# Optimization experiments

Hardware: AMD Instinct MI355X
Metric: run time of the kernel (lower is better)

The kernel has to match this reference:

```python
import jax, jax.numpy as jnp
import numpy as np

N, CS, CZ = 512, 384, 128
H, C, PQ, PV = 12, 16, 4, 8
NB = 8
EPS = 1e-8


def _ln(x, g, b):
    m = jnp.mean(x, axis=-1, keepdims=True)
    v = jnp.mean((x - m) ** 2, axis=-1, keepdims=True)
    return (x - m) / jnp.sqrt(v + 1e-5) * g + b


def _quat_rot(bcd):
    # (1, b, c, d) quaternion -> rotation matrix, as in AF2 BackboneUpdate
    ones = jnp.ones(bcd.shape[:-1] + (1,), bcd.dtype)
    q = jnp.concatenate([ones, bcd], axis=-1)
    q = q / jnp.linalg.norm(q, axis=-1, keepdims=True)
    w, x, y, z = q[..., 0], q[..., 1], q[..., 2], q[..., 3]
    R = jnp.stack([
        1 - 2 * (y * y + z * z), 2 * (x * y - w * z), 2 * (x * z + w * y),
        2 * (x * y + w * z), 1 - 2 * (x * x + z * z), 2 * (y * z - w * x),
        2 * (x * z - w * y), 2 * (y * z + w * x), 1 - 2 * (x * x + y * y),
    ], axis=-1)
    return R.reshape(bcd.shape[:-1] + (3, 3))


def _ipa(s, z, R, t, p):
    n = s.shape[0]
    q = (s @ p['w_q']).reshape(n, H, C)
    kv = (s @ p['w_kv']).reshape(n, H, 2, C)
    k, v = kv[..., 0, :], kv[..., 1, :]

    # local points -> global frames
    q_pts = (s @ p['w_qpts']).reshape(n, H * PQ, 3)
    q_pts = jnp.einsum('nxy,npy->npx', R, q_pts) + t[:, None, :]
    q_pts = q_pts.reshape(n, H, PQ, 3)
    kv_pts = (s @ p['w_kvpts']).reshape(n, H * (PQ + PV), 3)
    kv_pts = jnp.einsum('nxy,npy->npx', R, kv_pts) + t[:, None, :]
    kv_pts = kv_pts.reshape(n, H, PQ + PV, 3)
    k_pts, v_pts = kv_pts[:, :, :PQ], kv_pts[:, :, PQ:]

    b = z @ p['w_b']  # [i, j, H]

    scalar = jnp.einsum('ihc,jhc->hij', q, k) / np.sqrt(C)
    # sum_p ||q_ip - k_jp||^2 expanded to avoid [N,N,H,P,3] intermediate
    sq_q = jnp.sum(q_pts ** 2, axis=(-1, -2)).T  # [H, i]
    sq_k = jnp.sum(k_pts ** 2, axis=(-1, -2)).T  # [H, j]
    cross = jnp.einsum('ihpc,jhpc->hij', q_pts, k_pts)
    d2 = sq_q[:, :, None] + sq_k[:, None, :] - 2.0 * cross  # [H, i, j]

    gamma = jax.nn.softplus(p['head_weights'])  # [H]
    w_C = np.sqrt(2.0 / (9.0 * PQ))
    w_L = np.sqrt(1.0 / 3.0)
    logits = w_L * (scalar + jnp.transpose(b, (2, 0, 1))
                    - gamma[:, None, None] * (w_C / 2.0) * d2)
    a = jax.nn.softmax(logits, axis=-1)  # [H, i, j]

    o = jnp.einsum('hij,jhc->ihc', a, v).reshape(n, H * C)
    o_pt = jnp.einsum('hij,jhpc->ihpc', a, v_pts)
    # back to local frame: R_i^{-1} (o_pt - t_i)
    o_pt = jnp.einsum('nyx,nhpy->nhpx', R, o_pt - t[:, None, None, :])
    o_pt_norm = jnp.sqrt(jnp.sum(o_pt ** 2, axis=-1) + EPS)  # [n, H, PV]
    o_pair = jnp.einsum('hij,ijz->ihz', a, z).reshape(n, H * CZ)

    cat = jnp.concatenate([o, o_pt.reshape(n, H * PV * 3),
                           o_pt_norm.reshape(n, H * PV), o_pair], axis=-1)
    return cat @ p['w_out'] + p['b_out']


def _forward(s, z, p):
    n = s.shape[0]
    R = jnp.broadcast_to(jnp.eye(3, dtype=s.dtype), (n, 3, 3))
    t = jnp.zeros((n, 3), s.dtype)
    for _ in range(NB):  # shared weights across blocks, as in AF2
        s = s + _ipa(s, z, R, t, p)
        s = _ln(s, p['ln1_g'], p['ln1_b'])
        h = jax.nn.relu(s @ p['w_t1'])
        h = jax.nn.relu(h @ p['w_t2'])
        s = s + h @ p['w_t3']
        s = _ln(s, p['ln2_g'], p['ln2_b'])
        upd = s @ p['w_bb'] + p['b_bb']  # [n, 6]
        Ru = _quat_rot(upd[:, :3])
        tu = upd[:, 3:]
        t = jnp.einsum('nxy,ny->nx', R, tu) + t
        R = jnp.einsum('nxy,nyz->nxz', R, Ru)
    return jnp.concatenate([s, t], axis=-1)  # [n, CS + 3]


def setup_inputs() -> dict:
    key = jax.random.key(0)
    ks = jax.random.split(key, 12)
    sc = 0.02
    cat_dim = H * C + H * PV * 3 + H * PV + H * CZ  # 2112
    return {
        's': jax.random.normal(ks[0], (N, CS), jnp.float32),
        'z': jax.random.normal(ks[1], (N, N, CZ), jnp.float32),
        'w_q': jax.random.normal(ks[2], (CS, H * C), jnp.float32) * sc,
        'w_kv': jax.random.normal(ks[3], (CS, H * 2 * C), jnp.float32) * sc,
        'w_qpts': jax.random.normal(ks[4], (CS, H * PQ * 3), jnp.float32) * sc,
        'w_kvpts': jax.random.normal(ks[5], (CS, H * (PQ + PV) * 3), jnp.float32) * sc,
        'w_b': jax.random.normal(ks[6], (CZ, H), jnp.float32) * sc,
        'head_weights': jnp.zeros((H,), jnp.float32),
        'w_out': jax.random.normal(ks[7], (cat_dim, CS), jnp.float32) * sc,
        'b_out': jnp.zeros((CS,), jnp.float32),
        'ln1_g': jnp.ones((CS,), jnp.float32),
        'ln1_b': jnp.zeros((CS,), jnp.float32),
        'w_t1': jax.random.normal(ks[8], (CS, CS), jnp.float32) * sc,
        'w_t2': jax.random.normal(ks[9], (CS, CS), jnp.float32) * sc,
        'w_t3': jax.random.normal(ks[10], (CS, CS), jnp.float32) * sc,
        'ln2_g': jnp.ones((CS,), jnp.float32),
        'ln2_b': jnp.zeros((CS,), jnp.float32),
        'w_bb': jax.random.normal(ks[11], (CS, 6), jnp.float32) * sc,
        'b_bb': jnp.zeros((6,), jnp.float32),
    }


def reference(s, z, w_q, w_kv, w_qpts, w_kvpts, w_b, head_weights, w_out,
              b_out, ln1_g, ln1_b, w_t1, w_t2, w_t3, ln2_g, ln2_b, w_bb, b_bb):
    p = dict(w_q=w_q, w_kv=w_kv, w_qpts=w_qpts, w_kvpts=w_kvpts, w_b=w_b,
             head_weights=head_weights, w_out=w_out, b_out=b_out,
             ln1_g=ln1_g, ln1_b=ln1_b, w_t1=w_t1, w_t2=w_t2, w_t3=w_t3,
             ln2_g=ln2_g, ln2_b=ln2_b, w_bb=w_bb, b_bb=b_bb)
    return _forward(s, z, p)
```

## Files before the change

### kernel.cpp

```cpp
#include <hip/hip_runtime.h>
#include <hip/hip_bf16.h>

constexpr int Nres = 512;
constexpr int Cs   = 384;
constexpr int Cz   = 128;
constexpr int NH   = 12;
constexpr int HC   = 16;
constexpr int NPQ  = 4;
constexpr int NPV  = 8;
constexpr int NBLK = 8;
constexpr int PROJD = NH*HC + NH*2*HC + NH*NPQ*3 + NH*(NPQ+NPV)*3;
constexpr int CATD = NH*HC + NH*NPV*3 + NH*NPV + NH*Cz;
constexpr float W_L  = 0.57735026918962576f;
constexpr float W_C2 = 0.11785113019775793f;

using u16 = unsigned short;
typedef __bf16 bf16x8 __attribute__((ext_vector_type(8)));
typedef float  f32x4  __attribute__((ext_vector_type(4)));

static inline int gdiv(int n, int b) { return (n + b - 1) / b; }

static __device__ __forceinline__ u16 f2bf(float x) {
    __hip_bfloat16 h = __float2bfloat16(x);
    return *reinterpret_cast<u16*>(&h);
}
static __device__ __forceinline__ float bf2f(u16 x) {
    return __bfloat162float(*reinterpret_cast<__hip_bfloat16*>(&x));
}

__global__ void k_init(const float* __restrict__ s_in, float* __restrict__ s_cur,
                       u16* __restrict__ s_bf,
                       float* __restrict__ R, float* __restrict__ t) {
    int idx = blockIdx.x * blockDim.x + threadIdx.x;
    if (idx < Nres * Cs) { float v = s_in[idx]; s_cur[idx] = v; s_bf[idx] = f2bf(v); }
    if (idx < Nres * 9) {
        int e = idx % 9;
        R[idx] = (e == 0 || e == 4 || e == 8) ? 1.f : 0.f;
    }
    if (idx < Nres * 3) t[idx] = 0.f;
}

__global__ void k_concatW(const float* __restrict__ w_q, const float* __restrict__ w_kv,
                          const float* __restrict__ w_qpts, const float* __restrict__ w_kvpts,
                          float* __restrict__ Wcat) {
    int idx = blockIdx.x * blockDim.x + threadIdx.x;
    if (idx >= Cs * PROJD) return;
    int k = idx / PROJD, n = idx - k * PROJD;
    float v;
    if      (n < 192) v = w_q[k * 192 + n];
    else if (n < 576) v = w_kv[k * 384 + (n - 192)];
    else if (n < 720) v = w_qpts[k * 144 + (n - 576)];
    else              v = w_kvpts[k * 432 + (n - 720)];
    Wcat[idx] = v;
}

__global__ void k_transposeW(const float* __restrict__ in, u16* __restrict__ out,
                             int K, int N) {
    __shared__ float tile[32][33];
    int n0 = blockIdx.x * 32, k0 = blockIdx.y * 32;
    int tx = threadIdx.x & 31, ty = threadIdx.x >> 5;
#pragma unroll
    for (int j = 0; j < 4; j++)
        tile[ty + j * 8][tx] = in[(size_t)(k0 + ty + j * 8) * N + n0 + tx];
    __syncthreads();
#pragma unroll
    for (int j = 0; j < 4; j++)
        out[(size_t)(n0 + ty + j * 8) * K + k0 + tx] = f2bf(tile[tx][ty + j * 8]);
}

__global__ void k_zT(const float* __restrict__ z, u16* __restrict__ zT) {
    __shared__ float tile[32][33];
    int i  = blockIdx.x;
    int j0 = blockIdx.y * 32;
    int c0 = blockIdx.z * 32;
    int tx = threadIdx.x & 31, ty = threadIdx.x >> 5;
    const float* src = z + (size_t)i * Nres * Cz;
#pragma unroll
    for (int l = 0; l < 4; l++)
        tile[ty + l * 8][tx] = src[(size_t)(j0 + ty + l * 8) * Cz + c0 + tx];
    __syncthreads();
    u16* dst = zT + (size_t)i * Cz * Nres;
#pragma unroll
    for (int l = 0; l < 4; l++)
        dst[(size_t)(c0 + ty + l * 8) * Nres + j0 + tx] = f2bf(tile[tx][ty + l * 8]);
}

__global__ void __launch_bounds__(256)
k_gemm_mfma(const u16* __restrict__ A, const u16* __restrict__ Bt,
            float* __restrict__ P, int M, int K, int N, int Kc) {
    __shared__ u16 As[2][64 * 40];
    __shared__ u16 Bs[2][64 * 40];
    const int tid = threadIdx.x;
    const int m0 = blockIdx.y * 64;
    const int n0 = blockIdx.x * 64;
    const int kbeg = blockIdx.z * Kc;
    const int kend = kbeg + Kc;
    const int wv = tid >> 6, lane = tid & 63;
    const int wm = (wv >> 1) * 32, wn = (wv & 1) * 32;
    const int lrow = lane & 15, lq = lane >> 4;

    f32x4 zero = {0.f, 0.f, 0.f, 0.f};
    f32x4 acc00 = zero, acc01 = zero, acc10 = zero, acc11 = zero;

    const int srow = tid >> 2;
    const int sko  = (tid & 3) * 8;
    const size_t aoff = (size_t)(m0 + srow) * K + sko;
    const size_t boff = (size_t)(n0 + srow) * K + sko;

    uint4 ra = *(const uint4*)&A[aoff + kbeg];
    uint4 rb = *(const uint4*)&Bt[boff + kbeg];
    *(uint4*)&As[0][srow * 40 + sko] = ra;
    *(uint4*)&Bs[0][srow * 40 + sko] = rb;
    __syncthreads();

    int buf = 0;
    for (int k0 = kbeg; k0 < kend; k0 += 32) {
        const bool nxt = (k0 + 32 < kend);
        if (nxt) {
            ra = *(const uint4*)&A[aoff + k0 + 32];
            rb = *(const uint4*)&Bt[boff + k0 + 32];
        }
        bf16x8 a0 = *reinterpret_cast<const bf16x8*>(&As[buf][(wm + lrow) * 40 + lq * 8]);
        bf16x8 a1 = *reinterpret_cast<const bf16x8*>(&As[buf][(wm + 16 + lrow) * 40 + lq * 8]);
        bf16x8 b0 = *reinterpret_cast<const bf16x8*>(&Bs[buf][(wn + lrow) * 40 + lq * 8]);
        bf16x8 b1 = *reinterpret_cast<const bf16x8*>(&Bs[buf][(wn + 16 + lrow) * 40 + lq * 8]);
        acc00 = __builtin_amdgcn_mfma_f32_16x16x32_bf16(a0, b0, acc00, 0, 0, 0);
        acc01 = __builtin_amdgcn_mfma_f32_16x16x32_bf16(a0, b1, acc01, 0, 0, 0);
        acc10 = __builtin_amdgcn_mfma_f32_16x16x32_bf16(a1, b0, acc10, 0, 0, 0);
        acc11 = __builtin_amdgcn_mfma_f32_16x16x32_bf16(a1, b1, acc11, 0, 0, 0);
        if (nxt) {
            *(uint4*)&As[buf ^ 1][srow * 40 + sko] = ra;
            *(uint4*)&Bs[buf ^ 1][srow * 40 + sko] = rb;
            __syncthreads();
            buf ^= 1;
        }
    }
    float* Pp = P + (size_t)blockIdx.z * M * N;
    const int rbase = m0 + wm + lq * 4;
    const int cbase = n0 + wn + lrow;
#pragma unroll
    for (int r = 0; r < 4; r++) {
        Pp[(size_t)(rbase + r) * N + cbase]           = acc00[r];
        Pp[(size_t)(rbase + r) * N + cbase + 16]      = acc01[r];
        Pp[(size_t)(rbase + 16 + r) * N + cbase]      = acc10[r];
        Pp[(size_t)(rbase + 16 + r) * N + cbase + 16] = acc11[r];
    }
}

__global__ void __launch_bounds__(256)
k_gemm_proj(const u16* __restrict__ A, const u16* __restrict__ Bt,
            float* __restrict__ outT, int M, int K, int N) {
    __shared__ u16 As[2][32 * 40];
    __shared__ u16 Bs[2][64 * 40];
    const int tid = threadIdx.x;
    const int m0 = blockIdx.y * 32;
    const int n0 = blockIdx.x * 64;
    const int wv = tid >> 6, lane = tid & 63;
    const int wm = (wv >> 1) * 16, wn = (wv & 1) * 32;
    const int lrow = lane & 15, lq = lane >> 4;
    f32x4 zero = {0.f, 0.f, 0.f, 0.f};
    f32x4 acc0 = zero, acc1 = zero;
    const int srow = tid >> 2, sko = (tid & 3) * 8;
    const size_t aoff = (size_t)(m0 + srow) * K + sko;
    const size_t boff = (size_t)(n0 + srow) * K + sko;

    uint4 ra, rb;
    if (tid < 128) ra = *(const uint4*)&A[aoff];
    rb = *(const uint4*)&Bt[boff];
    if (tid < 128) *(uint4*)&As[0][srow * 40 + sko] = ra;
    *(uint4*)&Bs[0][srow * 40 + sko] = rb;
    __syncthreads();

    int buf = 0;
    for (int k0 = 0; k0 < K; k0 += 32) {
        const bool nxt = (k0 + 32 < K);
        if (nxt) {
            if (tid < 128) ra = *(const uint4*)&A[aoff + k0 + 32];
            rb = *(const uint4*)&Bt[boff + k0 + 32];
        }
        bf16x8 a  = *reinterpret_cast<const bf16x8*>(&As[buf][(wm + lrow) * 40 + lq * 8]);
        bf16x8 b0 = *reinterpret_cast<const bf16x8*>(&Bs[buf][(wn + lrow) * 40 + lq * 8]);
        bf16x8 b1 = *reinterpret_cast<const bf16x8*>(&Bs[buf][(wn + 16 + lrow) * 40 + lq * 8]);
        acc0 = __builtin_amdgcn_mfma_f32_16x16x32_bf16(a, b0, acc0, 0, 0, 0);
        acc1 = __builtin_amdgcn_mfma_f32_16x16x32_bf16(a, b1, acc1, 0, 0, 0);
        if (nxt) {
            if (tid < 128) *(uint4*)&As[buf ^ 1][srow * 40 + sko] = ra;
            *(uint4*)&Bs[buf ^ 1][srow * 40 + sko] = rb;
            __syncthreads();
            buf ^= 1;
        }
    }
    const int rbase = m0 + wm + lq * 4;
    const int cbase = n0 + wn + lrow;
    *reinterpret_cast<f32x4*>(&outT[(size_t)cbase * M + rbase])        = acc0;
    *reinterpret_cast<f32x4*>(&outT[(size_t)(cbase + 16) * M + rbase]) = acc1;
}

__global__ void __launch_bounds__(256)
k_gemm_tr(const u16* __restrict__ Abf, const float* __restrict__ As0,
          const float* __restrict__ As1, const u16* __restrict__ Bt,
          float* __restrict__ Pout, int amode) {
    __shared__ u16 Asm[2][32 * 40];
    __shared__ u16 Bsm[2][64 * 40];
    const int tid = threadIdx.x;
    const int m0 = blockIdx.y * 32;
    const int n0 = blockIdx.x * 64;
    const int kbeg = blockIdx.z * 192;
    const int kend = kbeg + 192;
    const int wv = tid >> 6, lane = tid & 63;
    const int wm = (wv >> 1) * 16, wn = (wv & 1) * 32;
    const int lrow = lane & 15, lq = lane >> 4;
    f32x4 zero = {0.f, 0.f, 0.f, 0.f};
    f32x4 acc0 = zero, acc1 = zero;
    const int srow = tid >> 2, sko = (tid & 3) * 8;
    const int rowR = tid >> 3, c4 = (tid & 7) * 4;
    const size_t aoffb = (size_t)(m0 + srow) * Cs + sko;
    const size_t aoffr = (size_t)(m0 + rowR) * Cs + c4;
    const size_t boff  = (size_t)(n0 + srow) * Cs + sko;

    uint4 ra, rb;
    float4 f0, f1;
    rb = *(const uint4*)&Bt[boff + kbeg];
    if (amode == 0) { if (tid < 128) ra = *(const uint4*)&Abf[aoffb + kbeg]; }
    else { f0 = *(const float4*)&As0[aoffr + kbeg]; f1 = *(const float4*)&As1[aoffr + kbeg]; }

    if (amode == 0) { if (tid < 128) *(uint4*)&Asm[0][srow * 40 + sko] = ra; }
    else {
        uint2 wp;
        wp.x = (unsigned)f2bf(fmaxf(f0.x + f1.x, 0.f)) | ((unsigned)f2bf(fmaxf(f0.y + f1.y, 0.f)) << 16);
        wp.y = (unsigned)f2bf(fmaxf(f0.z + f1.z, 0.f)) | ((unsigned)f2bf(fmaxf(f0.w + f1.w, 0.f)) << 16);
        *(uint2*)&Asm[0][rowR * 40 + c4] = wp;
    }
    *(uint4*)&Bsm[0][srow * 40 + sko] = rb;
    __syncthreads();

    int buf = 0;
    for (int k0 = kbeg; k0 < kend; k0 += 32) {
        const bool nxt = (k0 + 32 < kend);
        if (nxt) {
            rb = *(const uint4*)&Bt[boff + k0 + 32];
            if (amode == 0) { if (tid < 128) ra = *(const uint4*)&Abf[aoffb + k0 + 32]; }
            else { f0 = *(const float4*)&As0[aoffr + k0 + 32]; f1 = *(const float4*)&As1[aoffr + k0 + 32]; }
        }
        bf16x8 a  = *reinterpret_cast<const bf16x8*>(&Asm[buf][(wm + lrow) * 40 + lq * 8]);
        bf16x8 b0 = *reinterpret_cast<const bf16x8*>(&Bsm[buf][(wn + lrow) * 40 + lq * 8]);
        bf16x8 b1 = *reinterpret_cast<const bf16x8*>(&Bsm[buf][(wn + 16 + lrow) * 40 + lq * 8]);
        acc0 = __builtin_amdgcn_mfma_f32_16x16x32_bf16(a, b0, acc0, 0, 0, 0);
        acc1 = __builtin_amdgcn_mfma_f32_16x16x32_bf16(a, b1, acc1, 0, 0, 0);
        if (nxt) {
            if (amode == 0) { if (tid < 128) *(uint4*)&Asm[buf ^ 1][srow * 40 + sko] = ra; }
            else {
                uint2 wp;
                wp.x = (unsigned)f2bf(fmaxf(f0.x + f1.x, 0.f)) | ((unsigned)f2bf(fmaxf(f0.y + f1.y, 0.f)) << 16);
                wp.y = (unsigned)f2bf(fmaxf(f0.z + f1.z, 0.f)) | ((unsigned)f2bf(fmaxf(f0.w + f1.w, 0.f)) << 16);
                *(uint2*)&Asm[buf ^ 1][rowR * 40 + c4] = wp;
            }
            *(uint4*)&Bsm[buf ^ 1][srow * 40 + sko] = rb;
            __syncthreads();
            buf ^= 1;
        }
    }
    float* Pp = Pout + (size_t)blockIdx.z * Nres * Cs;
    const int rbase = m0 + wm + lq * 4;
    const int cbase = n0 + wn + lrow;
#pragma unroll
    for (int r = 0; r < 4; r++) {
        Pp[(size_t)(rbase + r) * Cs + cbase]      = acc0[r];
        Pp[(size_t)(rbase + r) * Cs + cbase + 16] = acc1[r];
    }
}

__global__ void k_bproj(const float* __restrict__ z, const float* __restrict__ w_b,
                        u16* __restrict__ b_hij_bf) {
    __shared__ float zs[16][129];
    __shared__ float wbs[Cz * NH];
    const int tid = threadIdx.x;
    const int base = blockIdx.x * 16;
#pragma unroll
    for (int l = 0; l < 6; l++) {
        int idx = tid + l * 256;
        if (idx < Cz * NH) wbs[idx] = w_b[idx];
    }
#pragma unroll
    for (int l = 0; l < 8; l++) {
        int idx = tid + l * 256;
        int r = idx >> 7, c = idx & 127;
        zs[r][c] = z[(size_t)(base + r) * Cz + c];
    }
    __syncthreads();
    if (tid < 192) {
        int h = tid >> 4, r = tid & 15;
        float acc = 0.f;
        for (int c = 0; c < Cz; c++) acc += zs[r][c] * wbs[c * NH + h];
        int row = base + r;
        int i = row >> 9, j = row & 511;
        b_hij_bf[((size_t)h * Nres + i) * Nres + j] = f2bf(acc * W_L);
    }
}

__global__ void k_prep(const float* __restrict__ projT, const float* __restrict__ R,
                       const float* __restrict__ t, const float* __restrict__ hw,
                       u16* __restrict__ Aaug, u16* __restrict__ Baug,
                       u16* __restrict__ vhT) {
    int idx = blockIdx.x * blockDim.x + threadIdx.x;
    if (idx >= NH * Nres) return;
    int h = idx / Nres, i = idx % Nres;
#define PR(col) projT[(size_t)(col) * Nres + i]
    float R_[9], t_[3];
#pragma unroll
    for (int e = 0; e < 9; e++) R_[e] = R[i * 9 + e];
#pragma unroll
    for (int e = 0; e < 3; e++) t_[e] = t[i * 3 + e];
    float gam = log1pf(__expf(hw[h]));
    float ch  = sqrtf(2.f * gam * W_C2);

    u16 arow[32], brow[32];
#pragma unroll
    for (int c = 0; c < HC; c++) {
        arow[c] = f2bf(PR(h * HC + c) * (W_L * 0.25f));
        brow[c] = f2bf(PR(192 + h * 2 * HC + c));
        vhT[((size_t)h * 48 + c) * Nres + i] = f2bf(PR(192 + h * 2 * HC + HC + c));
    }
#pragma unroll
    for (int p = 0; p < NPQ; p++) {
        int c0 = 576 + (h * NPQ + p) * 3;
        float y0 = PR(c0 + 0), y1 = PR(c0 + 1), y2 = PR(c0 + 2);
        float v0 = R_[0]*y0 + R_[1]*y1 + R_[2]*y2 + t_[0];
        float v1 = R_[3]*y0 + R_[4]*y1 + R_[5]*y2 + t_[1];
        float v2 = R_[6]*y0 + R_[7]*y1 + R_[8]*y2 + t_[2];
        float s = W_L * ch;
        arow[16 + p*3 + 0] = f2bf(v0 * s);
        arow[16 + p*3 + 1] = f2bf(v1 * s);
        arow[16 + p*3 + 2] = f2bf(v2 * s);
    }
    float sk = 0.f;
#pragma unroll
    for (int p = 0; p < NPQ + NPV; p++) {
        int c0 = 720 + (h * (NPQ+NPV) + p) * 3;
        float y0 = PR(c0 + 0), y1 = PR(c0 + 1), y2 = PR(c0 + 2);
        float v0 = R_[0]*y0 + R_[1]*y1 + R_[2]*y2 + t_[0];
        float v1 = R_[3]*y0 + R_[4]*y1 + R_[5]*y2 + t_[1];
        float v2 = R_[6]*y0 + R_[7]*y1 + R_[8]*y2 + t_[2];
        if (p < NPQ) {
            brow[16 + p*3 + 0] = f2bf(v0 * ch);
            brow[16 + p*3 + 1] = f2bf(v1 * ch);
            brow[16 + p*3 + 2] = f2bf(v2 * ch);
            sk += v0*v0 + v1*v1 + v2*v2;
        } else {
            int cc = 16 + (p - NPQ) * 3;
            vhT[((size_t)h * 48 + cc + 0) * Nres + i] = f2bf(v0);
            vhT[((size_t)h * 48 + cc + 1) * Nres + i] = f2bf(v1);
            vhT[((size_t)h * 48 + cc + 2) * Nres + i] = f2bf(v2);
        }
    }
#undef PR
    float x = -W_L * gam * W_C2 * sk;
    u16 hi = f2bf(x);
    float lo = x - bf2f(hi);
    arow[28] = f2bf(1.0f); arow[29] = f2bf(1.0f); arow[30] = 0; arow[31] = 0;
    brow[28] = hi;         brow[29] = f2bf(lo);   brow[30] = 0; brow[31] = 0;

    uint4* ad = (uint4*)&Aaug[((size_t)h * Nres + i) * 32];
    uint4* bd = (uint4*)&Baug[((size_t)h * Nres + i) * 32];
    const uint4* as = (const uint4*)arow;
    const uint4* bs = (const uint4*)brow;
#pragma unroll
    for (int e = 0; e < 4; e++) { ad[e] = as[e]; bd[e] = bs[e]; }
}

__global__ void __launch_bounds__(256)
k_attn(const u16* __restrict__ Aaug, const u16* __restrict__ Baug,
       const u16* __restrict__ b_hij_bf, const u16* __restrict__ vhT,
       const float* __restrict__ R, const float* __restrict__ t,
       u16* __restrict__ Pbf, u16* __restrict__ cat_bf) {
    __shared__ u16 P_lds[16 * 520];
    __shared__ float Ctp[4][16 * 49];
    __shared__ float sred[4][32];

    const int i0 = blockIdx.x * 16;
    const int h  = blockIdx.y;
    const int tid = threadIdx.x;
    const int w = tid >> 6, lane = tid & 63;
    const int lrow = lane & 15, lq = lane >> 4;
    const int jbase = w * 128;

    const u16* bhp = b_hij_bf + ((size_t)h * Nres + i0) * Nres;
    uint4 bhreg[4];
#pragma unroll
    for (int l = 0; l < 4; l++) {
        int v = tid + l * 256;
        int rr = v >> 6, cq = v & 63;
        bhreg[l] = *(const uint4*)&bhp[(size_t)rr * Nres + cq * 8];
    }

    bf16x8 afrag = *reinterpret_cast<const bf16x8*>(
        &Aaug[((size_t)h * Nres + i0 + lrow) * 32 + lq * 8]);
    f32x4 zero = {0.f, 0.f, 0.f, 0.f};
    f32x4 acc[8];
#pragma unroll
    for (int tt = 0; tt < 8; tt++) {
        bf16x8 bfr = *reinterpret_cast<const bf16x8*>(
            &Baug[((size_t)h * Nres + jbase + tt * 16 + lrow) * 32 + lq * 8]);
        acc[tt] = __builtin_amdgcn_mfma_f32_16x16x32_bf16(afrag, bfr, zero, 0, 0, 0);
    }

#pragma unroll
    for (int l = 0; l < 4; l++) {
        int v = tid + l * 256;
        int rr = v >> 6, cq = v & 63;
        *(uint4*)&P_lds[rr * 520 + cq * 8] = bhreg[l];
    }
    __syncthreads();
#pragma unroll
    for (int tt = 0; tt < 8; tt++)
#pragma unroll
        for (int r = 0; r < 4; r++)
            acc[tt][r] += bf2f(P_lds[(lq * 4 + r) * 520 + jbase + tt * 16 + lrow]);

    float pmx[4] = {-1e30f, -1e30f, -1e30f, -1e30f};
#pragma unroll
    for (int tt = 0; tt < 8; tt++)
#pragma unroll
        for (int r = 0; r < 4; r++) pmx[r] = fmaxf(pmx[r], acc[tt][r]);
#pragma unroll
    for (int off = 8; off > 0; off >>= 1)
#pragma unroll
        for (int r = 0; r < 4; r++) pmx[r] = fmaxf(pmx[r], __shfl_xor(pmx[r], off));
    if (lrow == 0) {
#pragma unroll
        for (int r = 0; r < 4; r++) sred[w][lq * 4 + r] = pmx[r];
    }
    __syncthreads();
    float mx[4];
#pragma unroll
    for (int r = 0; r < 4; r++) {
        int row = lq * 4 + r;
        mx[r] = fmaxf(fmaxf(sred[0][row], sred[1][row]), fmaxf(sred[2][row], sred[3][row]));
    }
    float psm[4] = {0.f, 0.f, 0.f, 0.f};
#pragma unroll
    for (int tt = 0; tt < 8; tt++)
#pragma unroll
        for (int r = 0; r < 4; r++) { acc[tt][r] = __expf(acc[tt][r] - mx[r]); psm[r] += acc[tt][r]; }
#pragma unroll
    for (int off = 8; off > 0; off >>= 1)
#pragma unroll
        for (int r = 0; r < 4; r++) psm[r] += __shfl_xor(psm[r], off);
    if (lrow == 0) {
#pragma unroll
        for (int r = 0; r < 4; r++) sred[w][16 + lq * 4 + r] = psm[r];
    }
    __syncthreads();
    float inv[4];
#pragma unroll
    for (int r = 0; r < 4; r++) {
        int row = 16 + lq * 4 + r;
        inv[r] = 1.f / (sred[0][row] + sred[1][row] + sred[2][row] + sred[3][row]);
    }

#pragma unroll
    for (int tt = 0; tt < 8; tt++)
#pragma unroll
        for (int r = 0; r < 4; r++)
            P_lds[(lq * 4 + r) * 520 + jbase + tt * 16 + lrow] = f2bf(acc[tt][r] * inv[r]);
    __syncthreads();

#pragma unroll
    for (int l = 0; l < 4; l++) {
        int v = tid + l * 256;
        int rr = v >> 6, cq = v & 63;
        *(uint4*)&Pbf[((size_t)h * Nres + i0 + rr) * 512 + cq * 8] =
            *(const uint4*)&P_lds[rr * 520 + cq * 8];
    }

    const u16* Bvp = vhT + (size_t)h * 48 * Nres;
    f32x4 o0 = zero, o1 = zero, o2 = zero;
#pragma unroll
    for (int s = 0; s < 4; s++) {
        int k0 = w * 128 + s * 32;
        bf16x8 a  = *reinterpret_cast<const bf16x8*>(&P_lds[lrow * 520 + k0 + lq * 8]);
        bf16x8 b0 = *reinterpret_cast<const bf16x8*>(&Bvp[(size_t)(lrow) * Nres + k0 + lq * 8]);
        bf16x8 b1 = *reinterpret_cast<const bf16x8*>(&Bvp[(size_t)(16 + lrow) * Nres + k0 + lq * 8]);
        bf16x8 b2 = *reinterpret_cast<const bf16x8*>(&Bvp[(size_t)(32 + lrow) * Nres + k0 + lq * 8]);
        o0 = __builtin_amdgcn_mfma_f32_16x16x32_bf16(a, b0, o0, 0, 0, 0);
        o1 = __builtin_amdgcn_mfma_f32_16x16x32_bf16(a, b1, o1, 0, 0, 0);
        o2 = __builtin_amdgcn_mfma_f32_16x16x32_bf16(a, b2, o2, 0, 0, 0);
    }
#pragma unroll
    for (int r = 0; r < 4; r++) {
        int row = lq * 4 + r;
        Ctp[w][row * 49 + lrow]      = o0[r];
        Ctp[w][row * 49 + 16 + lrow] = o1[r];
        Ctp[w][row * 49 + 32 + lrow] = o2[r];
    }
    __syncthreads();

    {
        int r = tid >> 4, c = tid & 15;
        float v = Ctp[0][r * 49 + c] + Ctp[1][r * 49 + c] + Ctp[2][r * 49 + c] + Ctp[3][r * 49 + c];
        cat_bf[(size_t)(i0 + r) * CATD + h * HC + c] = f2bf(v);
    }
    if (tid < 128) {
        int r = tid >> 3, p = tid & 7;
        int i = i0 + r;
        float g0 = 0.f, g1 = 0.f, g2 = 0.f;
#pragma unroll
        for (int ww = 0; ww < 4; ww++) {
            g0 += Ctp[ww][r * 49 + 16 + p * 3 + 0];
            g1 += Ctp[ww][r * 49 + 16 + p * 3 + 1];
            g2 += Ctp[ww][r * 49 + 16 + p * 3 + 2];
        }
        float d0 = g0 - t[i * 3 + 0], d1 = g1 - t[i * 3 + 1], d2v = g2 - t[i * 3 + 2];
        const float* Rn = R + i * 9;
        float l0 = Rn[0] * d0 + Rn[3] * d1 + Rn[6] * d2v;
        float l1 = Rn[1] * d0 + Rn[4] * d1 + Rn[7] * d2v;
        float l2 = Rn[2] * d0 + Rn[5] * d1 + Rn[8] * d2v;
        int hp = h * NPV + p;
        u16* crow = cat_bf + (size_t)i * CATD;
        crow[192 + hp * 3 + 0] = f2bf(l0);
        crow[192 + hp * 3 + 1] = f2bf(l1);
        crow[192 + hp * 3 + 2] = f2bf(l2);
        crow[480 + hp] = f2bf(sqrtf(l0 * l0 + l1 * l1 + l2 * l2 + 1e-8f));
    }
}

__global__ void __launch_bounds__(256)
k_opair(const u16* __restrict__ Pbf, const u16* __restrict__ zT,
        u16* __restrict__ cat_bf) {
    __shared__ u16 P_lds[16 * 520];
    __shared__ u16 Bs[2][128 * 40];
    const int i = blockIdx.x;
    const int tid = threadIdx.x;
    const int wv = tid >> 6, ln = tid & 63;
    const int srow = tid >> 2, sko = (tid & 3) * 8;
    const u16* Bp = zT + (size_t)i * Cz * Nres;
    const size_t b0off = (size_t)srow * Nres + sko;
    const size_t b1off = (size_t)(64 + srow) * Nres + sko;

    uint4 rb0 = *(const uint4*)&Bp[b0off];
    uint4 rb1 = *(const uint4*)&Bp[b1off];

#pragma unroll
    for (int l = 0; l < 3; l++) {
        int v = tid + l * 256;
        int hh = v >> 6, cq = v & 63;
        *(uint4*)&P_lds[hh * 520 + cq * 8] =
            *(const uint4*)&Pbf[((size_t)hh * Nres + i) * 512 + cq * 8];
    }
    for (int l = tid; l < 4 * 520; l += 256) P_lds[12 * 520 + l] = 0;

    *(uint4*)&Bs[0][srow * 40 + sko]        = rb0;
    *(uint4*)&Bs[0][(64 + srow) * 40 + sko] = rb1;
    __syncthreads();

    const int lrow = ln & 15, lq = ln >> 4;
    const int wn = wv * 32;
    f32x4 zero = {0.f, 0.f, 0.f, 0.f};
    f32x4 acc0 = zero, acc1 = zero;
    int buf = 0;
    for (int k0 = 0; k0 < Nres; k0 += 32) {
        const bool nxt = (k0 + 32 < Nres);
        if (nxt) {
            rb0 = *(const uint4*)&Bp[b0off + k0 + 32];
            rb1 = *(const uint4*)&Bp[b1off + k0 + 32];
        }
        bf16x8 a  = *reinterpret_cast<const bf16x8*>(&P_lds[lrow * 520 + k0 + lq * 8]);
        bf16x8 b0 = *reinterpret_cast<const bf16x8*>(&Bs[buf][(wn + lrow) * 40 + lq * 8]);
        bf16x8 b1 = *reinterpret_cast<const bf16x8*>(&Bs[buf][(wn + 16 + lrow) * 40 + lq * 8]);
        acc0 = __builtin_amdgcn_mfma_f32_16x16x32_bf16(a, b0, acc0, 0, 0, 0);
        acc1 = __builtin_amdgcn_mfma_f32_16x16x32_bf16(a, b1, acc1, 0, 0, 0);
        if (nxt) {
            *(uint4*)&Bs[buf ^ 1][srow * 40 + sko]        = rb0;
            *(uint4*)&Bs[buf ^ 1][(64 + srow) * 40 + sko] = rb1;
            __syncthreads();
            buf ^= 1;
        }
    }
    u16* crow = cat_bf + (size_t)i * CATD + 576;
#pragma unroll
    for (int r = 0; r < 4; r++) {
        int row = lq * 4 + r;
        if (row < NH) {
            crow[row * Cz + wn + lrow]      = f2bf(acc0[r]);
            crow[row * Cz + wn + 16 + lrow] = f2bf(acc1[r]);
        }
    }
}

__global__ void k_reduce_ln(const float* __restrict__ P, const float* __restrict__ bias,
                            float* __restrict__ s, u16* __restrict__ s_bf,
                            const float* __restrict__ g, const float* __restrict__ b,
                            int nsplit) {
    __shared__ float red[512];
    int i = blockIdx.x, tid = threadIdx.x;
    float v = s[(size_t)i * Cs + tid];
    if (bias) v += bias[tid];
    for (int sp = 0; sp < nsplit; sp++) v += P[(size_t)sp * Nres * Cs + (size_t)i * Cs + tid];
    red[tid] = v;
    if (tid < 128) red[384 + tid] = 0.f;
    __syncthreads();
    for (int st = 256; st > 0; st >>= 1) { if (tid < st) red[tid] += red[tid + st]; __syncthreads(); }
    float mean = red[0] / Cs;
    __syncthreads();
    float d = v - mean;
    red[tid] = d * d;
    if (tid < 128) red[384 + tid] = 0.f;
    __syncthreads();
    for (int st = 256; st > 0; st >>= 1) { if (tid < st) red[tid] += red[tid + st]; __syncthreads(); }
    float var = red[0] / Cs;
    float o = d * rsqrtf(var + 1e-5f) * g[tid] + b[tid];
    s[(size_t)i * Cs + tid] = o;
    s_bf[(size_t)i * Cs + tid] = f2bf(o);
}

__global__ void k_reduce_ln_bb(const float* __restrict__ P, float* __restrict__ s,
                               u16* __restrict__ s_bf,
                               const float* __restrict__ g, const float* __restrict__ b,
                               int nsplit,
                               const float* __restrict__ w_bb, const float* __restrict__ b_bb,
                               float* __restrict__ R, float* __restrict__ t,
                               float* __restrict__ outbuf) {
    __shared__ float red[512];
    __shared__ float uw[36];
    int i = blockIdx.x, tid = threadIdx.x;
    float v = s[(size_t)i * Cs + tid];
    for (int sp = 0; sp < nsplit; sp++) v += P[(size_t)sp * Nres * Cs + (size_t)i * Cs + tid];
    red[tid] = v;
    if (tid < 128) red[384 + tid] = 0.f;
    __syncthreads();
    for (int st = 256; st > 0; st >>= 1) { if (tid < st) red[tid] += red[tid + st]; __syncthreads(); }
    float mean = red[0] / Cs;
    __syncthreads();
    float d = v - mean;
    red[tid] = d * d;
    if (tid < 128) red[384 + tid] = 0.f;
    __syncthreads();
    for (int st = 256; st > 0; st >>= 1) { if (tid < st) red[tid] += red[tid + st]; __syncthreads(); }
    float var = red[0] / Cs;
    float o = d * rsqrtf(var + 1e-5f) * g[tid] + b[tid];
    s[(size_t)i * Cs + tid] = o;
    s_bf[(size_t)i * Cs + tid] = f2bf(o);
    if (outbuf) outbuf[(size_t)i * (Cs + 3) + tid] = o;

    float u[6];
#pragma unroll
    for (int dd = 0; dd < 6; dd++) u[dd] = o * w_bb[tid * 6 + dd];
#pragma unroll
    for (int off = 32; off > 0; off >>= 1)
#pragma unroll
        for (int dd = 0; dd < 6; dd++) u[dd] += __shfl_xor(u[dd], off);
    int wv = tid >> 6, lane = tid & 63;
    if (lane == 0) {
#pragma unroll
        for (int dd = 0; dd < 6; dd++) uw[wv * 6 + dd] = u[dd];
    }
    __syncthreads();
    if (tid == 0) {
        float uu[6];
#pragma unroll
        for (int dd = 0; dd < 6; dd++) {
            float a = b_bb[dd];
            for (int w = 0; w < 6; w++) a += uw[w * 6 + dd];
            uu[dd] = a;
        }
        float qb = uu[0], qc = uu[1], qd = uu[2];
        float inv = rsqrtf(1.f + qb*qb + qc*qc + qd*qd);
        float w = inv, x = qb * inv, y = qc * inv, zq = qd * inv;
        float Ru[9] = {
            1.f - 2.f*(y*y + zq*zq), 2.f*(x*y - w*zq),       2.f*(x*zq + w*y),
            2.f*(x*y + w*zq),        1.f - 2.f*(x*x + zq*zq), 2.f*(y*zq - w*x),
            2.f*(x*zq - w*y),        2.f*(y*zq + w*x),        1.f - 2.f*(x*x + y*y)
        };
        float Ro[9];
#pragma unroll
        for (int e = 0; e < 9; e++) Ro[e] = R[i * 9 + e];
        float tu0 = uu[3], tu1 = uu[4], tu2 = uu[5];
        float t0 = t[i*3+0] + Ro[0]*tu0 + Ro[1]*tu1 + Ro[2]*tu2;
        float t1 = t[i*3+1] + Ro[3]*tu0 + Ro[4]*tu1 + Ro[5]*tu2;
        float t2 = t[i*3+2] + Ro[6]*tu0 + Ro[7]*tu1 + Ro[8]*tu2;
        t[i*3+0] = t0; t[i*3+1] = t1; t[i*3+2] = t2;
        if (outbuf) {
            outbuf[(size_t)i * (Cs + 3) + Cs + 0] = t0;
            outbuf[(size_t)i * (Cs + 3) + Cs + 1] = t1;
            outbuf[(size_t)i * (Cs + 3) + Cs + 2] = t2;
        }
#pragma unroll
        for (int r = 0; r < 3; r++)
#pragma unroll
            for (int c = 0; c < 3; c++)
                R[i*9 + r*3 + c] = Ro[r*3+0]*Ru[0*3+c] + Ro[r*3+1]*Ru[1*3+c] + Ro[r*3+2]*Ru[2*3+c];
    }
}

extern "C" void kernel_launch(void* const* d_in, const int* in_sizes, int n_in,
                              void* d_out, int out_size, void* d_ws, size_t ws_size,
                              hipStream_t stream) {
    const float* s_in    = (const float*)d_in[0];
    const float* z       = (const float*)d_in[1];
    const float* w_q     = (const float*)d_in[2];
    const float* w_kv    = (const float*)d_in[3];
    const float* w_qpts  = (const float*)d_in[4];
    const float* w_kvpts = (const float*)d_in[5];
    const float* w_b     = (const float*)d_in[6];
    const float* hw      = (const float*)d_in[7];
    const float* w_out   = (const float*)d_in[8];
    const float* b_out   = (const float*)d_in[9];
    const float* ln1_g   = (const float*)d_in[10];
    const float* ln1_b   = (const float*)d_in[11];
    const float* w_t1    = (const float*)d_in[12];
    const float* w_t2    = (const float*)d_in[13];
    const float* w_t3    = (const float*)d_in[14];
    const float* ln2_g   = (const float*)d_in[15];
    const float* ln2_b   = (const float*)d_in[16];
    const float* w_bb    = (const float*)d_in[17];
    const float* b_bb    = (const float*)d_in[18];
    float* out = (float*)d_out;

    float* ws = (float*)d_ws;
    size_t off = 0;
    float* s_cur = ws + off; off += (size_t)Nres * Cs;
    float* projT = ws + off; off += (size_t)Nres * PROJD;
    float* Wcat  = ws + off; off += (size_t)Cs * PROJD;
    float* Rbuf  = ws + off; off += (size_t)Nres * 9;
    float* tbuf  = ws + off; off += (size_t)Nres * 3;
    float* Pslab = ws + off; off += (size_t)11 * Nres * Cs;
    u16* b_hij_bf = (u16*)(ws + off); off += (size_t)NH * Nres * Nres / 2;
    u16* s_bf   = (u16*)(ws + off); off += (size_t)Nres * Cs / 2;
    u16* cat_bf = (u16*)(ws + off); off += (size_t)Nres * CATD / 2;
    u16* WcatT  = (u16*)(ws + off); off += (size_t)Cs * PROJD / 2;
    u16* w_outT = (u16*)(ws + off); off += (size_t)CATD * Cs / 2;
    u16* w_t1T  = (u16*)(ws + off); off += (size_t)Cs * Cs / 2;
    u16* w_t2T  = (u16*)(ws + off); off += (size_t)Cs * Cs / 2;
    u16* w_t3T  = (u16*)(ws + off); off += (size_t)Cs * Cs / 2;
    u16* Pbf    = (u16*)(ws + off); off += (size_t)NH * Nres * Nres / 2;
    u16* vhTbf  = (u16*)(ws + off); off += (size_t)NH * 48 * Nres / 2;
    u16* Aaug   = (u16*)(ws + off); off += (size_t)NH * Nres * 32 / 2;
    u16* Baug   = (u16*)(ws + off); off += (size_t)NH * Nres * 32 / 2;
    u16* zTbf   = (u16*)(ws + off); off += (size_t)Nres * Cz * Nres / 2;

    const int MNs = Nres * Cs;

    k_init<<<gdiv(Nres*Cs, 256), 256, 0, stream>>>(s_in, s_cur, s_bf, Rbuf, tbuf);
    k_concatW<<<gdiv(Cs*PROJD, 256), 256, 0, stream>>>(w_q, w_kv, w_qpts, w_kvpts, Wcat);
    k_transposeW<<<dim3(PROJD/32, Cs/32), 256, 0, stream>>>(Wcat, WcatT, Cs, PROJD);
    k_transposeW<<<dim3(Cs/32, CATD/32), 256, 0, stream>>>(w_out, w_outT, CATD, Cs);
    k_transposeW<<<dim3(Cs/32, Cs/32), 256, 0, stream>>>(w_t1, w_t1T, Cs, Cs);
    k_transposeW<<<dim3(Cs/32, Cs/32), 256, 0, stream>>>(w_t2, w_t2T, Cs, Cs);
    k_transposeW<<<dim3(Cs/32, Cs/32), 256, 0, stream>>>(w_t3, w_t3T, Cs, Cs);
    k_bproj<<<Nres*Nres/16, 256, 0, stream>>>(z, w_b, b_hij_bf);
    k_zT<<<dim3(Nres, Nres/32, Cz/32), 256, 0, stream>>>(z, zTbf);

    for (int it = 0; it < NBLK; it++) {
        k_gemm_proj<<<dim3(PROJD/64, Nres/32), 256, 0, stream>>>(s_bf, WcatT, projT, Nres, Cs, PROJD);
        k_prep<<<gdiv(NH*Nres, 256), 256, 0, stream>>>(projT, Rbuf, tbuf, hw, Aaug, Baug, vhTbf);
        k_attn<<<dim3(Nres/16, NH), 256, 0, stream>>>(Aaug, Baug, b_hij_bf, vhTbf, Rbuf, tbuf, Pbf, cat_bf);
        k_opair<<<Nres, 256, 0, stream>>>(Pbf, zTbf, cat_bf);
        k_gemm_mfma<<<dim3(Cs/64, Nres/64, 6), 256, 0, stream>>>(cat_bf, w_outT, Pslab, Nres, CATD, Cs, 352);
        k_reduce_ln<<<Nres, Cs, 0, stream>>>(Pslab, b_out, s_cur, s_bf, ln1_g, ln1_b, 6);
        k_gemm_tr<<<dim3(Cs/64, Nres/32, 2), 256, 0, stream>>>(s_bf, nullptr, nullptr, w_t1T, Pslab, 0);
        k_gemm_tr<<<dim3(Cs/64, Nres/32, 2), 256, 0, stream>>>(nullptr, Pslab, Pslab + MNs, w_t2T, Pslab + 2*MNs, 1);
        k_gemm_tr<<<dim3(Cs/64, Nres/32, 2), 256, 0, stream>>>(nullptr, Pslab + 2*MNs, Pslab + 3*MNs, w_t3T, Pslab + 4*MNs, 1);
        k_reduce_ln_bb<<<Nres, Cs, 0, stream>>>(Pslab + 4*MNs, s_cur, s_bf, ln2_g, ln2_b, 2,
                                                w_bb, b_bb, Rbuf, tbuf,
                                                (it == NBLK - 1) ? out : nullptr);
    }
}
```

Baseline: 852.1 us.

## Raise split-K parallelism in projection, output and transition GEMMs

The projection GEMM is split along K into two slabs, and k_prep now sums them when reading. The separate 64x64 output GEMM and the two-slab transition GEMM are replaced by one generic split-K 32x64 kernel, k_gemm_sk. It runs the output projection in 11 K-chunks and each transition layer in 4, with the next layer summing four partial slabs inside its A-staging step. The aim is to launch many more blocks on these small GEMMs so the GPU is better filled, at the cost of more partial-sum memory traffic and extra adds in the reduce steps.

```diff
diff --git a/kernel.cpp b/kernel.cpp
--- a/kernel.cpp
+++ b/kernel.cpp
@@ -86,122 +86,10 @@
 }
 
 __global__ void __launch_bounds__(256)
-k_gemm_mfma(const u16* __restrict__ A, const u16* __restrict__ Bt,
-            float* __restrict__ P, int M, int K, int N, int Kc) {
-    __shared__ u16 As[2][64 * 40];
-    __shared__ u16 Bs[2][64 * 40];
-    const int tid = threadIdx.x;
-    const int m0 = blockIdx.y * 64;
-    const int n0 = blockIdx.x * 64;
-    const int kbeg = blockIdx.z * Kc;
-    const int kend = kbeg + Kc;
-    const int wv = tid >> 6, lane = tid & 63;
-    const int wm = (wv >> 1) * 32, wn = (wv & 1) * 32;
-    const int lrow = lane & 15, lq = lane >> 4;
-
-    f32x4 zero = {0.f, 0.f, 0.f, 0.f};
-    f32x4 acc00 = zero, acc01 = zero, acc10 = zero, acc11 = zero;
-
-    const int srow = tid >> 2;
-    const int sko  = (tid & 3) * 8;
-    const size_t aoff = (size_t)(m0 + srow) * K + sko;
-    const size_t boff = (size_t)(n0 + srow) * K + sko;
-
-    uint4 ra = *(const uint4*)&A[aoff + kbeg];
-    uint4 rb = *(const uint4*)&Bt[boff + kbeg];
-    *(uint4*)&As[0][srow * 40 + sko] = ra;
-    *(uint4*)&Bs[0][srow * 40 + sko] = rb;
-    __syncthreads();
-
-    int buf = 0;
-    for (int k0 = kbeg; k0 < kend; k0 += 32) {
-        const bool nxt = (k0 + 32 < kend);
-        if (nxt) {
-            ra = *(const uint4*)&A[aoff + k0 + 32];
-            rb = *(const uint4*)&Bt[boff + k0 + 32];
-        }
-        bf16x8 a0 = *reinterpret_cast<const bf16x8*>(&As[buf][(wm + lrow) * 40 + lq * 8]);
-        bf16x8 a1 = *reinterpret_cast<const bf16x8*>(&As[buf][(wm + 16 + lrow) * 40 + lq * 8]);
-        bf16x8 b0 = *reinterpret_cast<const bf16x8*>(&Bs[buf][(wn + lrow) * 40 + lq * 8]);
-        bf16x8 b1 = *reinterpret_cast<const bf16x8*>(&Bs[buf][(wn + 16 + lrow) * 40 + lq * 8]);
-        acc00 = __builtin_amdgcn_mfma_f32_16x16x32_bf16(a0, b0, acc00, 0, 0, 0);
-        acc01 = __builtin_amdgcn_mfma_f32_16x16x32_bf16(a0, b1, acc01, 0, 0, 0);
-        acc10 = __builtin_amdgcn_mfma_f32_16x16x32_bf16(a1, b0, acc10, 0, 0, 0);
-        acc11 = __builtin_amdgcn_mfma_f32_16x16x32_bf16(a1, b1, acc11, 0, 0, 0);
-        if (nxt) {
-            *(uint4*)&As[buf ^ 1][srow * 40 + sko] = ra;
-            *(uint4*)&Bs[buf ^ 1][srow * 40 + sko] = rb;
-            __syncthreads();
-            buf ^= 1;
-        }
-    }
-    float* Pp = P + (size_t)blockIdx.z * M * N;
-    const int rbase = m0 + wm + lq * 4;
-    const int cbase = n0 + wn + lrow;
-#pragma unroll
-    for (int r = 0; r < 4; r++) {
-        Pp[(size_t)(rbase + r) * N + cbase]           = acc00[r];
-        Pp[(size_t)(rbase + r) * N + cbase + 16]      = acc01[r];
-        Pp[(size_t)(rbase + 16 + r) * N + cbase]      = acc10[r];
-        Pp[(size_t)(rbase + 16 + r) * N + cbase + 16] = acc11[r];
-    }
-}
-
-__global__ void __launch_bounds__(256)
 k_gemm_proj(const u16* __restrict__ A, const u16* __restrict__ Bt,
             float* __restrict__ outT, int M, int K, int N) {
     __shared__ u16 As[2][32 * 40];
     __shared__ u16 Bs[2][64 * 40];
-    const int tid = threadIdx.x;
-    const int m0 = blockIdx.y * 32;
-    const int n0 = blockIdx.x * 64;
-    const int wv = tid >> 6, lane = tid & 63;
-    const int wm = (wv >> 1) * 16, wn = (wv & 1) * 32;
-    const int lrow = lane & 15, lq = lane >> 4;
-    f32x4 zero = {0.f, 0.f, 0.f, 0.f};
-    f32x4 acc0 = zero, acc1 = zero;
-    const int srow = tid >> 2, sko = (tid & 3) * 8;
-    const size_t aoff = (size_t)(m0 + srow) * K + sko;
-    const size_t boff = (size_t)(n0 + srow) * K + sko;
-
-    uint4 ra, rb;
-    if (tid < 128) ra = *(const uint4*)&A[aoff];
-    rb = *(const uint4*)&Bt[boff];
-    if (tid < 128) *(uint4*)&As[0][srow * 40 + sko] = ra;
-    *(uint4*)&Bs[0][srow * 40 + sko] = rb;
-    __syncthreads();
-
-    int buf = 0;
-    for (int k0 = 0; k0 < K; k0 += 32) {
-        const bool nxt = (k0 + 32 < K);
-        if (nxt) {
-            if (tid < 128) ra = *(const uint4*)&A[aoff + k0 + 32];
-            rb = *(const uint4*)&Bt[boff + k0 + 32];
-        }
-        bf16x8 a  = *reinterpret_cast<const bf16x8*>(&As[buf][(wm + lrow) * 40 + lq * 8]);
-        bf16x8 b0 = *reinterpret_cast<const bf16x8*>(&Bs[buf][(wn + lrow) * 40 + lq * 8]);
-        bf16x8 b1 = *reinterpret_cast<const bf16x8*>(&Bs[buf][(wn + 16 + lrow) * 40 + lq * 8]);
-        acc0 = __builtin_amdgcn_mfma_f32_16x16x32_bf16(a, b0, acc0, 0, 0, 0);
-        acc1 = __builtin_amdgcn_mfma_f32_16x16x32_bf16(a, b1, acc1, 0, 0, 0);
-        if (nxt) {
-            if (tid < 128) *(uint4*)&As[buf ^ 1][srow * 40 + sko] = ra;
-            *(uint4*)&Bs[buf ^ 1][srow * 40 + sko] = rb;
-            __syncthreads();
-            buf ^= 1;
-        }
-    }
-    const int rbase = m0 + wm + lq * 4;
-    const int cbase = n0 + wn + lrow;
-    *reinterpret_cast<f32x4*>(&outT[(size_t)cbase * M + rbase])        = acc0;
-    *reinterpret_cast<f32x4*>(&outT[(size_t)(cbase + 16) * M + rbase]) = acc1;
-}
-
-__global__ void __launch_bounds__(256)
-k_gemm_tr(const u16* __restrict__ Abf, const float* __restrict__ As0,
-          const float* __restrict__ As1, const u16* __restrict__ Bt,
-          float* __restrict__ Pout, int amode) {
-    __shared__ u16 Asm[2][32 * 40];
-    __shared__ u16 Bsm[2][64 * 40];
     const int tid = threadIdx.x;
     const int m0 = blockIdx.y * 32;
     const int n0 = blockIdx.x * 64;
@@ -213,24 +101,91 @@
     f32x4 zero = {0.f, 0.f, 0.f, 0.f};
     f32x4 acc0 = zero, acc1 = zero;
     const int srow = tid >> 2, sko = (tid & 3) * 8;
+    const size_t aoff = (size_t)(m0 + srow) * K + sko;
+    const size_t boff = (size_t)(n0 + srow) * K + sko;
+
+    uint4 ra, rb;
+    if (tid < 128) ra = *(const uint4*)&A[aoff + kbeg];
+    rb = *(const uint4*)&Bt[boff + kbeg];
+    if (tid < 128) *(uint4*)&As[0][srow * 40 + sko] = ra;
+    *(uint4*)&Bs[0][srow * 40 + sko] = rb;
+    __syncthreads();
+
+    int buf = 0;
+    for (int k0 = kbeg; k0 < kend; k0 += 32) {
+        const bool nxt = (k0 + 32 < kend);
+        if (nxt) {
+            if (tid < 128) ra = *(const uint4*)&A[aoff + k0 + 32];
+            rb = *(const uint4*)&Bt[boff + k0 + 32];
+        }
+        bf16x8 a  = *reinterpret_cast<const bf16x8*>(&As[buf][(wm + lrow) * 40 + lq * 8]);
+        bf16x8 b0 = *reinterpret_cast<const bf16x8*>(&Bs[buf][(wn + lrow) * 40 + lq * 8]);
+        bf16x8 b1 = *reinterpret_cast<const bf16x8*>(&Bs[buf][(wn + 16 + lrow) * 40 + lq * 8]);
+        acc0 = __builtin_amdgcn_mfma_f32_16x16x32_bf16(a, b0, acc0, 0, 0, 0);
+        acc1 = __builtin_amdgcn_mfma_f32_16x16x32_bf16(a, b1, acc1, 0, 0, 0);
+        if (nxt) {
+            if (tid < 128) *(uint4*)&As[buf ^ 1][srow * 40 + sko] = ra;
+            *(uint4*)&Bs[buf ^ 1][srow * 40 + sko] = rb;
+            __syncthreads();
+            buf ^= 1;
+        }
+    }
+    float* op = outT + (size_t)blockIdx.z * N * M;
+    const int rbase = m0 + wm + lq * 4;
+    const int cbase = n0 + wn + lrow;
+    *reinterpret_cast<f32x4*>(&op[(size_t)cbase * M + rbase])        = acc0;
+    *reinterpret_cast<f32x4*>(&op[(size_t)(cbase + 16) * M + rbase]) = acc1;
+}
+
+__global__ void __launch_bounds__(256)
+k_gemm_sk(const u16* __restrict__ Abf, const float* __restrict__ Aslab,
+          const u16* __restrict__ Bt, float* __restrict__ Pout,
+          int K, int Kc) {
+    __shared__ u16 Asm[2][32 * 40];
+    __shared__ u16 Bsm[2][64 * 40];
+    const int tid = threadIdx.x;
+    const int m0 = blockIdx.y * 32;
+    const int n0 = blockIdx.x * 64;
+    const int kbeg = blockIdx.z * Kc;
+    const int kend = kbeg + Kc;
+    const int wv = tid >> 6, lane = tid & 63;
+    const int wm = (wv >> 1) * 16, wn = (wv & 1) * 32;
+    const int lrow = lane & 15, lq = lane >> 4;
+    f32x4 zero = {0.f, 0.f, 0.f, 0.f};
+    f32x4 acc0 = zero, acc1 = zero;
+    const int srow = tid >> 2, sko = (tid & 3) * 8;
     const int rowR = tid >> 3, c4 = (tid & 7) * 4;
-    const size_t aoffb = (size_t)(m0 + srow) * Cs + sko;
-    const size_t aoffr = (size_t)(m0 + rowR) * Cs + c4;
-    const size_t boff  = (size_t)(n0 + srow) * Cs + sko;
+    const size_t aoffb = (size_t)(m0 + srow) * K + sko;
+    const size_t aoffr = (size_t)(m0 + rowR) * K + c4;
+    const size_t boff  = (size_t)(n0 + srow) * K + sko;
+    constexpr size_t SL = (size_t)Nres * Cs;
 
     uint4 ra, rb;
-    float4 f0, f1;
+    float4 f0, f1, f2, f3;
     rb = *(const uint4*)&Bt[boff + kbeg];
-    if (amode == 0) { if (tid < 128) ra = *(const uint4*)&Abf[aoffb + kbeg]; }
-    else { f0 = *(const float4*)&As0[aoffr + kbeg]; f1 = *(const float4*)&As1[aoffr + kbeg]; }
-
-    if (amode == 0) { if (tid < 128) *(uint4*)&Asm[0][srow * 40 + sko] = ra; }
+    if (Aslab == nullptr) { if (tid < 128) ra = *(const uint4*)&Abf[aoffb + kbeg]; }
     else {
-        uint2 wp;
-        wp.x = (unsigned)f2bf(fmaxf(f0.x + f1.x, 0.f)) | ((unsigned)f2bf(fmaxf(f0.y + f1.y, 0.f)) << 16);
-        wp.y = (unsigned)f2bf(fmaxf(f0.z + f1.z, 0.f)) | ((unsigned)f2bf(fmaxf(f0.w + f1.w, 0.f)) << 16);
-        *(uint2*)&Asm[0][rowR * 40 + c4] = wp;
-    }
+        f0 = *(const float4*)&Aslab[aoffr + kbeg];
+        f1 = *(const float4*)&Aslab[SL + aoffr + kbeg];
+        f2 = *(const float4*)&Aslab[2*SL + aoffr + kbeg];
+        f3 = *(const float4*)&Aslab[3*SL + aoffr + kbeg];
+    }
+
+#define STAGE_A(b)                                                              \
+    if (Aslab == nullptr) {                                                     \
+        if (tid < 128) *(uint4*)&Asm[b][srow * 40 + sko] = ra;                  \
+    } else {                                                                    \
+        float x0 = fmaxf(f0.x + f1.x + f2.x + f3.x, 0.f);                       \
+        float x1 = fmaxf(f0.y + f1.y + f2.y + f3.y, 0.f);                       \
+        float x2 = fmaxf(f0.z + f1.z + f2.z + f3.z, 0.f);                       \
+        float x3 = fmaxf(f0.w + f1.w + f2.w + f3.w, 0.f);                       \
+        uint2 wp;                                                               \
+        wp.x = (unsigned)f2bf(x0) | ((unsigned)f2bf(x1) << 16);                 \
+        wp.y = (unsigned)f2bf(x2) | ((unsigned)f2bf(x3) << 16);                 \
+        *(uint2*)&Asm[b][rowR * 40 + c4] = wp;                                  \
+    }
+
+    STAGE_A(0);
     *(uint4*)&Bsm[0][srow * 40 + sko] = rb;
     __syncthreads();
 
@@ -239,8 +194,13 @@
         const bool nxt = (k0 + 32 < kend);
         if (nxt) {
             rb = *(const uint4*)&Bt[boff + k0 + 32];
-            if (amode == 0) { if (tid < 128) ra = *(const uint4*)&Abf[aoffb + k0 + 32]; }
-            else { f0 = *(const float4*)&As0[aoffr + k0 + 32]; f1 = *(const float4*)&As1[aoffr + k0 + 32]; }
+            if (Aslab == nullptr) { if (tid < 128) ra = *(const uint4*)&Abf[aoffb + k0 + 32]; }
+            else {
+                f0 = *(const float4*)&Aslab[aoffr + k0 + 32];
+                f1 = *(const float4*)&Aslab[SL + aoffr + k0 + 32];
+                f2 = *(const float4*)&Aslab[2*SL + aoffr + k0 + 32];
+                f3 = *(const float4*)&Aslab[3*SL + aoffr + k0 + 32];
+            }
         }
         bf16x8 a  = *reinterpret_cast<const bf16x8*>(&Asm[buf][(wm + lrow) * 40 + lq * 8]);
         bf16x8 b0 = *reinterpret_cast<const bf16x8*>(&Bsm[buf][(wn + lrow) * 40 + lq * 8]);
@@ -248,19 +208,14 @@
         acc0 = __builtin_amdgcn_mfma_f32_16x16x32_bf16(a, b0, acc0, 0, 0, 0);
         acc1 = __builtin_amdgcn_mfma_f32_16x16x32_bf16(a, b1, acc1, 0, 0, 0);
         if (nxt) {
-            if (amode == 0) { if (tid < 128) *(uint4*)&Asm[buf ^ 1][srow * 40 + sko] = ra; }
-            else {
-                uint2 wp;
-                wp.x = (unsigned)f2bf(fmaxf(f0.x + f1.x, 0.f)) | ((unsigned)f2bf(fmaxf(f0.y + f1.y, 0.f)) << 16);
-                wp.y = (unsigned)f2bf(fmaxf(f0.z + f1.z, 0.f)) | ((unsigned)f2bf(fmaxf(f0.w + f1.w, 0.f)) << 16);
-                *(uint2*)&Asm[buf ^ 1][rowR * 40 + c4] = wp;
-            }
+            STAGE_A(buf ^ 1);
             *(uint4*)&Bsm[buf ^ 1][srow * 40 + sko] = rb;
             __syncthreads();
             buf ^= 1;
         }
     }
-    float* Pp = Pout + (size_t)blockIdx.z * Nres * Cs;
+#undef STAGE_A
+    float* Pp = Pout + (size_t)blockIdx.z * SL;
     const int rbase = m0 + wm + lq * 4;
     const int cbase = n0 + wn + lrow;
 #pragma unroll
@@ -305,7 +260,8 @@
     int idx = blockIdx.x * blockDim.x + threadIdx.x;
     if (idx >= NH * Nres) return;
     int h = idx / Nres, i = idx % Nres;
-#define PR(col) projT[(size_t)(col) * Nres + i]
+    constexpr size_t PSL = (size_t)PROJD * Nres;
+#define PR(col) (projT[(size_t)(col) * Nres + i] + projT[PSL + (size_t)(col) * Nres + i])
     float R_[9], t_[3];
 #pragma unroll
     for (int e = 0; e < 9; e++) R_[e] = R[i * 9 + e];
@@ -719,11 +675,11 @@
     float* ws = (float*)d_ws;
     size_t off = 0;
     float* s_cur = ws + off; off += (size_t)Nres * Cs;
-    float* projT = ws + off; off += (size_t)Nres * PROJD;
+    float* projT = ws + off; off += (size_t)2 * Nres * PROJD;
     float* Wcat  = ws + off; off += (size_t)Cs * PROJD;
     float* Rbuf  = ws + off; off += (size_t)Nres * 9;
     float* tbuf  = ws + off; off += (size_t)Nres * 3;
-    float* Pslab = ws + off; off += (size_t)11 * Nres * Cs;
+    float* Pslab = ws + off; off += (size_t)12 * Nres * Cs;
     u16* b_hij_bf = (u16*)(ws + off); off += (size_t)NH * Nres * Nres / 2;
     u16* s_bf   = (u16*)(ws + off); off += (size_t)Nres * Cs / 2;
     u16* cat_bf = (u16*)(ws + off); off += (size_t)Nres * CATD / 2;
@@ -738,7 +694,7 @@
     u16* Baug   = (u16*)(ws + off); off += (size_t)NH * Nres * 32 / 2;
     u16* zTbf   = (u16*)(ws + off); off += (size_t)Nres * Cz * Nres / 2;
 
-    const int MNs = Nres * Cs;
+    const size_t MNs = (size_t)Nres * Cs;
 
     k_init<<<gdiv(Nres*Cs, 256), 256, 0, stream>>>(s_in, s_cur, s_bf, Rbuf, tbuf);
     k_concatW<<<gdiv(Cs*PROJD, 256), 256, 0, stream>>>(w_q, w_kv, w_qpts, w_kvpts, Wcat);
@@ -751,16 +707,16 @@
     k_zT<<<dim3(Nres, Nres/32, Cz/32), 256, 0, stream>>>(z, zTbf);
 
     for (int it = 0; it < NBLK; it++) {
-        k_gemm_proj<<<dim3(PROJD/64, Nres/32), 256, 0, stream>>>(s_bf, WcatT, projT, Nres, Cs, PROJD);
+        k_gemm_proj<<<dim3(PROJD/64, Nres/32, 2), 256, 0, stream>>>(s_bf, WcatT, projT, Nres, Cs, PROJD);
         k_prep<<<gdiv(NH*Nres, 256), 256, 0, stream>>>(projT, Rbuf, tbuf, hw, Aaug, Baug, vhTbf);
         k_attn<<<dim3(Nres/16, NH), 256, 0, stream>>>(Aaug, Baug, b_hij_bf, vhTbf, Rbuf, tbuf, Pbf, cat_bf);
         k_opair<<<Nres, 256, 0, stream>>>(Pbf, zTbf, cat_bf);
-        k_gemm_mfma<<<dim3(Cs/64, Nres/64, 6), 256, 0, stream>>>(cat_bf, w_outT, Pslab, Nres, CATD, Cs, 352);
-        k_reduce_ln<<<Nres, Cs, 0, stream>>>(Pslab, b_out, s_cur, s_bf, ln1_g, ln1_b, 6);
-        k_gemm_tr<<<dim3(Cs/64, Nres/32, 2), 256, 0, stream>>>(s_bf, nullptr, nullptr, w_t1T, Pslab, 0);
-        k_gemm_tr<<<dim3(Cs/64, Nres/32, 2), 256, 0, stream>>>(nullptr, Pslab, Pslab + MNs, w_t2T, Pslab + 2*MNs, 1);
-        k_gemm_tr<<<dim3(Cs/64, Nres/32, 2), 256, 0, stream>>>(nullptr, Pslab + 2*MNs, Pslab + 3*MNs, w_t3T, Pslab + 4*MNs, 1);
-        k_reduce_ln_bb<<<Nres, Cs, 0, stream>>>(Pslab + 4*MNs, s_cur, s_bf, ln2_g, ln2_b, 2,
+        k_gemm_sk<<<dim3(Cs/64, Nres/32, 11), 256, 0, stream>>>(cat_bf, nullptr, w_outT, Pslab, CATD, 192);
+        k_reduce_ln<<<Nres, Cs, 0, stream>>>(Pslab, b_out, s_cur, s_bf, ln1_g, ln1_b, 11);
+        k_gemm_sk<<<dim3(Cs/64, Nres/32, 4), 256, 0, stream>>>(s_bf, nullptr, w_t1T, Pslab, Cs, 96);
+        k_gemm_sk<<<dim3(Cs/64, Nres/32, 4), 256, 0, stream>>>(nullptr, Pslab, w_t2T, Pslab + 4*MNs, Cs, 96);
+        k_gemm_sk<<<dim3(Cs/64, Nres/32, 4), 256, 0, stream>>>(nullptr, Pslab + 4*MNs, w_t3T, Pslab + 8*MNs, Cs, 96);
+        k_reduce_ln_bb<<<Nres, Cs, 0, stream>>>(Pslab + 8*MNs, s_cur, s_bf, ln2_g, ln2_b, 4,
                                                 w_bb, b_bb, Rbuf, tbuf,
                                                 (it == NBLK - 1) ? out : nullptr);
     }
```

Result: slower. 869.5 us (+2.0%).
